# Kernel optimization log

Measured on AMD Instinct MI355X. Metric: run time of the kernel, lower is better.

Reference implementation:

```python
import jax, jax.numpy as jnp
import numpy as np


def _conv(x, w, b, stride):
    y = jax.lax.conv_general_dilated(x, w, (stride, stride), [(1, 1), (1, 1)],
                                     dimension_numbers=('NCHW', 'OIHW', 'NCHW'))
    return y + b[None, :, None, None]


def _prelu(x, a):
    return jnp.where(x >= 0, x, a[None, :, None, None] * x)


def _conv2_block(x, wa, ba, aa, wb, bb, ab):
    # conv2 = stride-2 conv + PReLU, then stride-1 conv + PReLU (RIFE-style)
    x = _prelu(_conv(x, wa, ba, 2), aa)
    return _prelu(_conv(x, wb, bb, 1), ab)


def _halve_flow(flow):
    # F.interpolate(scale_factor=0.5, bilinear, align_corners=False) on exact
    # half-downsampling == 2x2 average pooling; then * 0.5 rescales flow units.
    B, C, H, W = flow.shape
    return flow.reshape(B, C, H // 2, 2, W // 2, 2).mean(axis=(3, 5)) * 0.5


def _splat_one(inp, flow):
    # inp [C,H,W], flow [2,H,W]: bilinear forward-splat (scatter-add) summation
    C, H, W = inp.shape
    gx = jnp.arange(W, dtype=flow.dtype)
    gy = jnp.arange(H, dtype=flow.dtype)
    fx = flow[0] + gx[None, :]  # target x coord per source pixel
    fy = flow[1] + gy[:, None]
    x0 = jnp.floor(fx); y0 = jnp.floor(fy)
    x1 = x0 + 1.0;      y1 = y0 + 1.0
    src = inp.reshape(C, H * W)
    out = jnp.zeros((C, H * W), inp.dtype)
    corners = [(x0, y0, (x1 - fx) * (y1 - fy)),
               (x1, y0, (fx - x0) * (y1 - fy)),
               (x0, y1, (x1 - fx) * (fy - y0)),
               (x1, y1, (fx - x0) * (fy - y0))]
    for xi, yi, w in corners:
        valid = (xi >= 0) & (xi < W) & (yi >= 0) & (yi < H)
        idx = yi.astype(jnp.int32) * W + xi.astype(jnp.int32)
        idx = jnp.where(valid, idx, 0).reshape(-1)
        wv = jnp.where(valid, w, 0.0).reshape(-1)
        out = out.at[:, idx].add(src * wv[None, :])
    return out.reshape(C, H, W)


def _softsplat_avg(inp, flow):
    # strType='average': splat features and a ones channel, divide by count
    num = jax.vmap(_splat_one)(inp, flow)
    cnt = jax.vmap(_splat_one)(jnp.ones_like(inp[:, :1]), flow)
    return num / jnp.where(cnt == 0.0, 1.0, cnt)


def setup_inputs() -> dict:
    key = jax.random.key(0)
    ks = jax.random.split(key, 12)
    B, H, W = 16, 512, 512
    d = {
        'img': jax.random.normal(ks[0], (B, 3, H, W), jnp.float32),
        'flow': jax.random.normal(ks[1], (B, 2, H, W), jnp.float32) * 4.0,
    }
    c = 16
    chans = [(3, c), (c, 2 * c), (2 * c, 4 * c), (4 * c, 8 * c)]
    for i, (ci, co) in enumerate(chans, start=1):
        ka, kb = jax.random.split(ks[1 + i], 2)
        d[f'w{i}a'] = jax.random.normal(ka, (co, ci, 3, 3), jnp.float32) * 0.1
        d[f'b{i}a'] = jnp.zeros((co,), jnp.float32)
        d[f'a{i}a'] = jnp.full((co,), 0.25, jnp.float32)
        d[f'w{i}b'] = jax.random.normal(kb, (co, co, 3, 3), jnp.float32) * 0.1
        d[f'b{i}b'] = jnp.zeros((co,), jnp.float32)
        d[f'a{i}b'] = jnp.full((co,), 0.25, jnp.float32)
    return d


def reference(img, flow,
              w1a, b1a, a1a, w1b, b1b, a1b,
              w2a, b2a, a2a, w2b, b2b, a2b,
              w3a, b3a, a3a, w3b, b3b, a3b,
              w4a, b4a, a4a, w4b, b4b, a4b):
    blocks = [(w1a, b1a, a1a, w1b, b1b, a1b),
              (w2a, b2a, a2a, w2b, b2b, a2b),
              (w3a, b3a, a3a, w3b, b3b, a3b),
              (w4a, b4a, a4a, w4b, b4b, a4b)]
    feat = img
    fl = flow
    pyr = []
    for blk in blocks:
        feat = _conv2_block(feat, *blk)
        fl = _halve_flow(fl)
        pyr.append(_softsplat_avg(feat, fl))
    return tuple(pyr)
```

## Files before the change

### kernel.cpp

```cpp
#include <hip/hip_runtime.h>

#define CDIV(a, b) (((a) + (b) - 1) / (b))

typedef float __attribute__((ext_vector_type(2))) f32x2;
typedef float __attribute__((ext_vector_type(4))) f32x4;

__device__ __forceinline__ void pk_fma(f32x2& d, f32x2 a, f32x2 b) {
    asm("v_pk_fma_f32 %0, %1, %2, %0" : "+v"(d) : "v"(a), "v"(b));
}

__device__ __forceinline__ void fadd_native(float* p, float v) {
    unsafeAtomicAdd(p, v);
}

template <int STRIDE, int TW, int TH, int CB>
__global__ __launch_bounds__(256)
void conv3x3_pk_kernel(const float* __restrict__ in,
                       const float* __restrict__ wgt,
                       const float* __restrict__ bias,
                       const float* __restrict__ alpha,
                       float* __restrict__ out,
                       int Ci, int Hi, int Wi, int Co, int Ho, int Wo,
                       int nTX) {
    constexpr int KO  = 16;
    constexpr int PX  = TW / 16, PY = TH / 16;
    constexpr int ISX = TW * STRIDE + 2;
    constexpr int ISY = TH * STRIDE + 2;
    constexpr int ISS = ISX * ISY;
    constexpr int NST = (CB * ISS + 255) / 256;
    constexpr int NWT = (CB * 9 * KO + 255) / 256;
    __shared__ float s_in[CB * ISS];
    __shared__ __align__(16) float s_wt[CB * 9 * KO];

    const int b   = blockIdx.z;
    const int co0 = blockIdx.y * KO;
    const int tX  = (blockIdx.x % nTX) * TW;
    const int tY  = (blockIdx.x / nTX) * TH;
    const int t   = threadIdx.x;
    const int tcx = t & 15, tcy = t >> 4;
    const int ox0 = PX * tcx, oy0 = PY * tcy;
    const int HiWi = Hi * Wi;

    int  poff[NST];
    bool pval[NST];
    const int ix0 = tX * STRIDE - 1, iy0 = tY * STRIDE - 1;
#pragma unroll
    for (int s = 0; s < NST; ++s) {
        const int i = t + s * 256;
        int off = 0; bool v = false;
        if (i < CB * ISS) {
            const int p = i / ISS, j = i - p * ISS;
            const int r = j / ISX, c = j - r * ISX;
            const int gy = iy0 + r, gx = ix0 + c;
            v = (gy >= 0) && (gy < Hi) && (gx >= 0) && (gx < Wi);
            off = v ? (p * HiWi + gy * Wi + gx) : 0;
        }
        poff[s] = off; pval[s] = v;
    }
    int  wofs[NWT], wdst[NWT];
    bool wvs[NWT];
#pragma unroll
    for (int s = 0; s < NWT; ++s) {
        const int j = t + s * 256;
        bool v = j < CB * 9 * KO;
        int ofs = 0, dst = 0;
        if (v) {
            const int p = j / (9 * KO), rem = j - p * 9 * KO;
            const int k = rem / KO, ko = rem - k * KO;
            ofs = ((co0 + ko) * Ci + p) * 9 + k;
            dst = (p * 9 + k) * KO + ko;
        }
        wofs[s] = ofs; wdst[s] = dst; wvs[s] = v;
    }

    f32x2 acc2[KO / 2][PY][PX];
#pragma unroll
    for (int cp = 0; cp < KO / 2; ++cp)
#pragma unroll
        for (int dy = 0; dy < PY; ++dy)
#pragma unroll
            for (int dx = 0; dx < PX; ++dx) acc2[cp][dy][dx] = (f32x2){0.f, 0.f};

    const float* inb = in + (size_t)b * Ci * HiWi;

    float rs[NST], rw[NWT];
#pragma unroll
    for (int s = 0; s < NST; ++s) rs[s] = pval[s] ? inb[poff[s]] : 0.f;
#pragma unroll
    for (int s = 0; s < NWT; ++s) rw[s] = wvs[s] ? wgt[wofs[s]] : 0.f;

    const int bx = ox0 * STRIDE, by = oy0 * STRIDE;

    for (int ci = 0; ci < Ci; ci += CB) {
        __syncthreads();
#pragma unroll
        for (int s = 0; s < NST; ++s) {
            const int i = t + s * 256;
            if (i < CB * ISS) s_in[i] = rs[s];
        }
#pragma unroll
        for (int s = 0; s < NWT; ++s)
            if (wvs[s]) s_wt[wdst[s]] = rw[s];
        if (ci + CB < Ci) {
            const float* nb = inb + (size_t)(ci + CB) * HiWi;
            const int w9 = (ci + CB) * 9;
#pragma unroll
            for (int s = 0; s < NST; ++s) rs[s] = pval[s] ? nb[poff[s]] : 0.f;
#pragma unroll
            for (int s = 0; s < NWT; ++s)
                rw[s] = wvs[s] ? wgt[wofs[s] + w9] : 0.f;
        }
        __syncthreads();

#pragma unroll
        for (int p = 0; p < CB; ++p) {
            const float* sp = s_in + p * ISS;
#pragma unroll
            for (int ky = 0; ky < 3; ++ky)
#pragma unroll
                for (int kx = 0; kx < 3; ++kx) {
                    const int k = ky * 3 + kx;
                    f32x2 t2[PY][PX];
#pragma unroll
                    for (int dy = 0; dy < PY; ++dy)
#pragma unroll
                        for (int dx = 0; dx < PX; ++dx) {
                            const float tv =
                                sp[(by + dy * STRIDE + ky) * ISX + bx +
                                   dx * STRIDE + kx];
                            t2[dy][dx] = (f32x2){tv, tv};
                        }
                    const float* wb = s_wt + (p * 9 + k) * KO;
#pragma unroll
                    for (int kq = 0; kq < KO / 4; ++kq) {
                        const f32x4 w4 =
                            *reinterpret_cast<const f32x4*>(wb + 4 * kq);
                        const f32x2 wlo = {w4[0], w4[1]};
                        const f32x2 whi = {w4[2], w4[3]};
#pragma unroll
                        for (int dy = 0; dy < PY; ++dy)
#pragma unroll
                            for (int dx = 0; dx < PX; ++dx) {
                                pk_fma(acc2[2 * kq][dy][dx], t2[dy][dx], wlo);
                                pk_fma(acc2[2 * kq + 1][dy][dx], t2[dy][dx], whi);
                            }
                    }
                }
        }
    }

#pragma unroll
    for (int cp = 0; cp < KO / 2; ++cp)
#pragma unroll
        for (int h = 0; h < 2; ++h) {
            const int co = co0 + 2 * cp + h;
            const float bv = bias[co], av = alpha[co];
#pragma unroll
            for (int dy = 0; dy < PY; ++dy) {
                const int oy = tY + oy0 + dy;
#pragma unroll
                for (int dx = 0; dx < PX; ++dx) {
                    const int ox = tX + ox0 + dx;
                    float v = acc2[cp][dy][dx][h] + bv;
                    v = v >= 0.f ? v : av * v;
                    out[(((size_t)b * Co + co) * Ho + oy) * Wo + ox] = v;
                }
            }
        }
}

__global__ void halve_flow_kernel(const float* __restrict__ in,
                                  float* __restrict__ out,
                                  int BC, int Ho, int Wo, int Hi, int Wi) {
    const int idx = blockIdx.x * blockDim.x + threadIdx.x;
    const int total = BC * Ho * Wo;
    if (idx >= total) return;
    const int wo = idx % Wo;
    int t = idx / Wo;
    const int ho = t % Ho;
    const int bc = t / Ho;
    const float* p = in + ((size_t)bc * Hi + 2 * ho) * Wi + 2 * wo;
    out[idx] = (p[0] + p[1] + p[Wi] + p[Wi + 1]) * 0.125f;
}

__global__ void splat_outlier_kernel(const float* __restrict__ feat,
                                     const float* __restrict__ flow,
                                     float* __restrict__ num,
                                     float* __restrict__ cnt,
                                     int* __restrict__ flag,
                                     int B, int C, int H, int W, float thr) {
    const int HW = H * W;
    const int idx = blockIdx.x * blockDim.x + threadIdx.x;
    if (idx >= B * HW) return;
    const int b = idx / HW, px = idx - b * HW;
    const int y = px / W, x = px - y * W;
    const float dx = flow[(size_t)b * 2 * HW + px];
    const float dy = flow[(size_t)b * 2 * HW + HW + px];
    if (fabsf(dx) <= thr && fabsf(dy) <= thr) return;
    atomicAdd(flag, 1);
    const float fx = dx + (float)x, fy = dy + (float)y;
    const float x0f = floorf(fx), y0f = floorf(fy);
    const int x0 = (int)x0f, y0 = (int)y0f;
    const float ax = fx - x0f, ay = fy - y0f;
    const float w[4] = {(1.f - ax) * (1.f - ay), ax * (1.f - ay),
                        (1.f - ax) * ay,         ax * ay};
    const int cx[4] = {x0, x0 + 1, x0, x0 + 1};
    const int cy[4] = {y0, y0, y0 + 1, y0 + 1};
    float* cb = cnt + (size_t)b * HW;
    for (int k = 0; k < 4; ++k) {
        if (cx[k] < 0 || cx[k] >= W || cy[k] < 0 || cy[k] >= H) continue;
        if (w[k] == 0.f) continue;
        const size_t d = (size_t)cy[k] * W + cx[k];
        fadd_native(cb + d, w[k]);
        for (int c = 0; c < C; ++c)
            fadd_native(num + ((size_t)b * C + c) * HW + d,
                        feat[((size_t)b * C + c) * HW + px] * w[k]);
    }
}

template <int TS, int K, int NCH, int HCAP>
__global__ __launch_bounds__(256)
void splat_gather_kernel(const float* __restrict__ feat,
                         const float* __restrict__ flow,
                         const float* __restrict__ cnt_ov,
                         const int* __restrict__ oflag,
                         float* __restrict__ out,
                         int C, int H, int W, int nTX) {
    constexpr int WS   = TS + 2 * K;
    constexpr int SSTR = WS + 1;
    constexpr int RUN  = TS * TS / 256;
    constexpr int TPR  = TS / RUN;
    constexpr float THR = (float)(K - 1);
    __shared__ float s_fx[WS * SSTR];
    __shared__ float s_fy[WS * SSTR];
    __shared__ unsigned short s_hit[256 * HCAP];

    const int b   = blockIdx.z;
    const int c0  = blockIdx.y * NCH;
    const int tx0 = (blockIdx.x % nTX) * TS;
    const int ty0 = (blockIdx.x / nTX) * TS;
    const int t   = threadIdx.x;
    const int HW  = H * W;
    const float* flx = flow + (size_t)b * 2 * HW;
    const float* fly = flx + HW;
    const float* fb  = feat + ((size_t)b * C + c0) * HW;

    for (int i = t; i < WS * WS; i += 256) {
        const int wsy = i / WS, wsx = i - wsy * WS;
        const int gy = ty0 - K + wsy, gx = tx0 - K + wsx;
        float fxr = 1e9f, fyr = 1e9f;
        if (gy >= 0 && gy < H && gx >= 0 && gx < W) {
            const float dxf = flx[(size_t)gy * W + gx];
            const float dyf = fly[(size_t)gy * W + gx];
            if (fabsf(dxf) <= THR && fabsf(dyf) <= THR) {
                fxr = dxf + (float)(gx - tx0);
                fyr = dyf + (float)(gy - ty0);
            }
        }
        s_fx[wsy * SSTR + wsx] = fxr;
        s_fy[wsy * SSTR + wsx] = fyr;
    }
    __syncthreads();

    const int r  = t / TPR;
    const int x0 = (t % TPR) * RUN;

    int n = 0;
    unsigned short* hl = s_hit + t * HCAP;
#pragma unroll
    for (int dy = 0; dy <= 2 * K; ++dy) {
        const int wsy = r + dy;
        const int base = wsy * SSTR + x0;
#pragma unroll
        for (int dxx = 0; dxx < RUN + 2 * K; ++dxx) {
            const float fyr = s_fy[base + dxx];
            const float fxr = s_fx[base + dxx];
            const float ty = fyr - (float)r;
            const float ux = fxr - (float)x0;
            if (ty > -1.f && ty < 1.f && ux > -1.f && ux < (float)RUN &&
                n < HCAP) {
                hl[n] = (unsigned short)((wsy << 6) | (x0 + dxx));
                ++n;
            }
        }
    }

    float acc[RUN][NCH];
    float cnt[RUN];
#pragma unroll
    for (int m = 0; m < RUN; ++m) {
        cnt[m] = 0.f;
#pragma unroll
        for (int ch = 0; ch < NCH; ++ch) acc[m][ch] = 0.f;
    }

    for (int k = 0; k < n; ++k) {
        const int idx = hl[k];
        const int wsy = idx >> 6, wsx = idx & 63;
        const float fxr = s_fx[wsy * SSTR + wsx];
        const float fyr = s_fy[wsy * SSTR + wsx];
        const float wy = 1.f - fabsf(fyr - (float)r);
        const float ux = fxr - (float)x0;
        const int gsy = ty0 - K + wsy, gsx = tx0 - K + wsx;
        const float* fp = fb + (size_t)gsy * W + gsx;
        float wm[RUN];
#pragma unroll
        for (int m = 0; m < RUN; ++m) {
            wm[m] = fmaxf(0.f, 1.f - fabsf(ux - (float)m)) * wy;
            cnt[m] += wm[m];
        }
#pragma unroll
        for (int ch = 0; ch < NCH; ++ch) {
            const float f = fp[(size_t)ch * HW];
#pragma unroll
            for (int m = 0; m < RUN; ++m)
                acc[m][ch] = fmaf(wm[m], f, acc[m][ch]);
        }
    }

    const int has = *oflag;
    const int gy = ty0 + r;
    const size_t rowoff = (size_t)gy * W + (tx0 + x0);
    float inv[RUN];
#pragma unroll
    for (int m = 0; m < RUN; ++m) {
        float cv = cnt[m];
        if (has) cv += cnt_ov[(size_t)b * HW + rowoff + m];
        inv[m] = 1.f / ((cv == 0.f) ? 1.f : cv);
    }
#pragma unroll
    for (int ch = 0; ch < NCH; ++ch) {
        const size_t go = ((size_t)b * C + (c0 + ch)) * HW + rowoff;
        if constexpr (RUN == 4) {
            float vv[4];
#pragma unroll
            for (int m = 0; m < 4; ++m) {
                float x = acc[m][ch];
                if (has) x += out[go + m];
                vv[m] = x * inv[m];
            }
            float4 v4 = {vv[0], vv[1], vv[2], vv[3]};
            *reinterpret_cast<float4*>(out + go) = v4;
        } else {
            float x = acc[0][ch];
            if (has) x += out[go];
            out[go] = x * inv[0];
        }
    }
}

extern "C" void kernel_launch(void* const* d_in, const int* in_sizes, int n_in,
                              void* d_out, int out_size, void* d_ws, size_t ws_size,
                              hipStream_t stream) {
    (void)in_sizes; (void)n_in; (void)ws_size;

    const float* img  = (const float*)d_in[0];
    const float* flow = (const float*)d_in[1];
    const float* P[4][6];
    for (int i = 0; i < 4; ++i)
        for (int j = 0; j < 6; ++j)
            P[i][j] = (const float*)d_in[2 + 6 * i + j];

    const int Bn = 16;
    float* ws = (float*)d_ws;
    float* bufA = ws;
    float* bufB = ws + 16777216;
    float* flA  = ws + 33554432;
    float* flB  = ws + 35651584;
    float* cnt  = ws + 36175872;
    int*   flag = (int*)(ws + 37224448);
    float* out  = (float*)d_out;

    hipMemsetAsync(d_out, 0, (size_t)out_size * sizeof(float), stream);

    auto halve = [&](const float* in, float* o, int Hi, int Wi) {
        const int Ho = Hi / 2, Wo = Wi / 2;
        const int total = Bn * 2 * Ho * Wo;
        hipLaunchKernelGGL(halve_flow_kernel, dim3(CDIV(total, 256)), dim3(256),
                           0, stream, in, o, Bn * 2, Ho, Wo, Hi, Wi);
    };

    float* p1 = out;
    float* p2 = p1 + (size_t)Bn * 16 * 256 * 256;
    float* p3 = p2 + (size_t)Bn * 32 * 128 * 128;
    float* p4 = p3 + (size_t)Bn * 64 * 64 * 64;

#define CONV(S, TWv, THv, CBv, inp, wi, o, Ci_, Hi_, Wi_, Co_)                 \
    do {                                                                       \
        const int Ho_ = (Hi_) / (S), Wo_ = (Wi_) / (S);                        \
        const int nTX_ = Wo_ / (TWv), nTY_ = Ho_ / (THv);                      \
        hipLaunchKernelGGL((conv3x3_pk_kernel<S, TWv, THv, CBv>),              \
                           dim3(nTX_ * nTY_, (Co_) / 16, Bn), dim3(256), 0,    \
                           stream, inp, P[wi][0 + 3 * ((S) == 1)],             \
                           P[wi][1 + 3 * ((S) == 1)], P[wi][2 + 3 * ((S) == 1)],\
                           o, Ci_, Hi_, Wi_, Co_, Ho_, Wo_, nTX_);             \
    } while (0)

    CONV(2, 32, 32, 1, img,  0, bufA, 3, 512, 512, 16);
    CONV(1, 32, 32, 2, bufA, 0, bufB, 16, 256, 256, 16);
    halve(flow, flA, 512, 512);
    {
        const int C = 16, H = 256, W = 256;
        hipMemsetAsync(cnt, 0, (size_t)Bn * H * W * sizeof(float), stream);
        hipMemsetAsync(flag, 0, sizeof(int), stream);
        hipLaunchKernelGGL(splat_outlier_kernel, dim3(CDIV(Bn * H * W, 256)),
                           dim3(256), 0, stream, bufB, flA, p1, cnt, flag,
                           Bn, C, H, W, 3.f);
        hipLaunchKernelGGL((splat_gather_kernel<32, 4, 16, 40>),
                           dim3((W / 32) * (H / 32), C / 16, Bn), dim3(256), 0,
                           stream, bufB, flA, cnt, flag, p1, C, H, W, W / 32);
    }

    CONV(2, 32, 32, 1, bufB, 1, bufA, 16, 256, 256, 32);
    CONV(1, 32, 32, 2, bufA, 1, bufB, 32, 128, 128, 32);
    halve(flA, flB, 256, 256);
    {
        const int C = 32, H = 128, W = 128;
        hipMemsetAsync(cnt, 0, (size_t)Bn * H * W * sizeof(float), stream);
        hipMemsetAsync(flag, 0, sizeof(int), stream);
        hipLaunchKernelGGL(splat_outlier_kernel, dim3(CDIV(Bn * H * W, 256)),
                           dim3(256), 0, stream, bufB, flB, p2, cnt, flag,
                           Bn, C, H, W, 2.f);
        hipLaunchKernelGGL((splat_gather_kernel<32, 3, 16, 40>),
                           dim3((W / 32) * (H / 32), C / 16, Bn), dim3(256), 0,
                           stream, bufB, flB, cnt, flag, p2, C, H, W, W / 32);
    }

    CONV(2, 32, 16, 1, bufB, 2, bufA, 32, 128, 128, 64);
    CONV(1, 32, 16, 2, bufA, 2, bufB, 64, 64, 64, 64);
    halve(flB, flA, 128, 128);
    {
        const int C = 64, H = 64, W = 64;
        hipMemsetAsync(cnt, 0, (size_t)Bn * H * W * sizeof(float), stream);
        hipMemsetAsync(flag, 0, sizeof(int), stream);
        hipLaunchKernelGGL(splat_outlier_kernel, dim3(CDIV(Bn * H * W, 256)),
                           dim3(256), 0, stream, bufB, flA, p3, cnt, flag,
                           Bn, C, H, W, 1.f);
        hipLaunchKernelGGL((splat_gather_kernel<16, 2, 16, 24>),
                           dim3((W / 16) * (H / 16), C / 16, Bn), dim3(256), 0,
                           stream, bufB, flA, cnt, flag, p3, C, H, W, W / 16);
    }

    CONV(2, 16, 16, 1, bufB, 3, bufA, 64, 64, 64, 128);
    CONV(1, 16, 16, 2, bufA, 3, bufB, 128, 32, 32, 128);
    halve(flA, flB, 64, 64);
    {
        const int C = 128, H = 32, W = 32;
        hipMemsetAsync(cnt, 0, (size_t)Bn * H * W * sizeof(float), stream);
        hipMemsetAsync(flag, 0, sizeof(int), stream);
        hipLaunchKernelGGL(splat_outlier_kernel, dim3(CDIV(Bn * H * W, 256)),
                           dim3(256), 0, stream, bufB, flB, p4, cnt, flag,
                           Bn, C, H, W, 1.f);
        hipLaunchKernelGGL((splat_gather_kernel<16, 2, 16, 24>),
                           dim3((W / 16) * (H / 16), C / 16, Bn), dim3(256), 0,
                           stream, bufB, flB, cnt, flag, p4, C, H, W, W / 16);
    }
#undef CONV
}
```

Before: 1.173 ms.

## Stage feature tiles in LDS per channel and drop global outlier flag

The gather splat kernel now loads each channel's feature window into shared memory, double-buffered through registers with a prefetch of the next channel. It then accumulates per channel from LDS rather than issuing scattered global loads for every hit and channel. Flow x/y are packed into one interleaved float2 shared array, the global atomic outlier flag is replaced by a per-pixel check on the count value, and hit-list capacities are reduced. This trades register-heavy accumulators for two barriers per channel and a redo of the hit-list loop for each channel.

```diff
diff --git a/kernel.cpp b/kernel.cpp
--- a/kernel.cpp
+++ b/kernel.cpp
@@ -187,7 +187,6 @@
                                      const float* __restrict__ flow,
                                      float* __restrict__ num,
                                      float* __restrict__ cnt,
-                                     int* __restrict__ flag,
                                      int B, int C, int H, int W, float thr) {
     const int HW = H * W;
     const int idx = blockIdx.x * blockDim.x + threadIdx.x;
@@ -197,7 +196,6 @@
     const float dx = flow[(size_t)b * 2 * HW + px];
     const float dy = flow[(size_t)b * 2 * HW + HW + px];
     if (fabsf(dx) <= thr && fabsf(dy) <= thr) return;
-    atomicAdd(flag, 1);
     const float fx = dx + (float)x, fy = dy + (float)y;
     const float x0f = floorf(fx), y0f = floorf(fy);
     const int x0 = (int)x0f, y0 = (int)y0f;
@@ -220,19 +218,19 @@
 
 template <int TS, int K, int NCH, int HCAP>
 __global__ __launch_bounds__(256)
-void splat_gather_kernel(const float* __restrict__ feat,
-                         const float* __restrict__ flow,
-                         const float* __restrict__ cnt_ov,
-                         const int* __restrict__ oflag,
-                         float* __restrict__ out,
-                         int C, int H, int W, int nTX) {
+void splat_gather2_kernel(const float* __restrict__ feat,
+                          const float* __restrict__ flow,
+                          const float* __restrict__ cnt_ov,
+                          float* __restrict__ out,
+                          int C, int H, int W, int nTX) {
     constexpr int WS   = TS + 2 * K;
     constexpr int SSTR = WS + 1;
     constexpr int RUN  = TS * TS / 256;
     constexpr int TPR  = TS / RUN;
+    constexpr int NSF  = (WS * WS + 255) / 256;
     constexpr float THR = (float)(K - 1);
-    __shared__ float s_fx[WS * SSTR];
-    __shared__ float s_fy[WS * SSTR];
+    __shared__ __align__(8) float s_xy[2 * WS * SSTR];
+    __shared__ float s_feat[WS * SSTR];
     __shared__ unsigned short s_hit[256 * HCAP];
 
     const int b   = blockIdx.z;
@@ -245,20 +243,30 @@
     const float* fly = flx + HW;
     const float* fb  = feat + ((size_t)b * C + c0) * HW;
 
-    for (int i = t; i < WS * WS; i += 256) {
-        const int wsy = i / WS, wsx = i - wsy * WS;
-        const int gy = ty0 - K + wsy, gx = tx0 - K + wsx;
-        float fxr = 1e9f, fyr = 1e9f;
-        if (gy >= 0 && gy < H && gx >= 0 && gx < W) {
-            const float dxf = flx[(size_t)gy * W + gx];
-            const float dyf = fly[(size_t)gy * W + gx];
-            if (fabsf(dxf) <= THR && fabsf(dyf) <= THR) {
-                fxr = dxf + (float)(gx - tx0);
-                fyr = dyf + (float)(gy - ty0);
-            }
-        }
-        s_fx[wsy * SSTR + wsx] = fxr;
-        s_fy[wsy * SSTR + wsx] = fyr;
+    int  foff[NSF], sdst[NSF];
+    bool fval[NSF];
+#pragma unroll
+    for (int s = 0; s < NSF; ++s) {
+        const int i = t + s * 256;
+        foff[s] = 0; sdst[s] = 0; fval[s] = false;
+        if (i < WS * WS) {
+            const int wsy = i / WS, wsx = i - wsy * WS;
+            const int gy = ty0 - K + wsy, gx = tx0 - K + wsx;
+            const int off = wsy * SSTR + wsx;
+            sdst[s] = off;
+            float fxr = 1e9f, fyr = 1e9f;
+            if (gy >= 0 && gy < H && gx >= 0 && gx < W) {
+                fval[s] = true;
+                foff[s] = gy * W + gx;
+                const float dxf = flx[foff[s]];
+                const float dyf = fly[foff[s]];
+                if (fabsf(dxf) <= THR && fabsf(dyf) <= THR) {
+                    fxr = dxf + (float)(gx - tx0);
+                    fyr = dyf + (float)(gy - ty0);
+                }
+            }
+            *reinterpret_cast<f32x2*>(&s_xy[2 * off]) = (f32x2){fxr, fyr};
+        }
     }
     __syncthreads();
 
@@ -273,10 +281,10 @@
         const int base = wsy * SSTR + x0;
 #pragma unroll
         for (int dxx = 0; dxx < RUN + 2 * K; ++dxx) {
-            const float fyr = s_fy[base + dxx];
-            const float fxr = s_fx[base + dxx];
-            const float ty = fyr - (float)r;
-            const float ux = fxr - (float)x0;
+            const f32x2 xy =
+                *reinterpret_cast<const f32x2*>(&s_xy[2 * (base + dxx)]);
+            const float ty = xy[1] - (float)r;
+            const float ux = xy[0] - (float)x0;
             if (ty > -1.f && ty < 1.f && ux > -1.f && ux < (float)RUN &&
                 n < HCAP) {
                 hl[n] = (unsigned short)((wsy << 6) | (x0 + dxx));
@@ -285,65 +293,71 @@
         }
     }
 
-    float acc[RUN][NCH];
-    float cnt[RUN];
-#pragma unroll
-    for (int m = 0; m < RUN; ++m) {
-        cnt[m] = 0.f;
-#pragma unroll
-        for (int ch = 0; ch < NCH; ++ch) acc[m][ch] = 0.f;
-    }
-
-    for (int k = 0; k < n; ++k) {
-        const int idx = hl[k];
-        const int wsy = idx >> 6, wsx = idx & 63;
-        const float fxr = s_fx[wsy * SSTR + wsx];
-        const float fyr = s_fy[wsy * SSTR + wsx];
-        const float wy = 1.f - fabsf(fyr - (float)r);
-        const float ux = fxr - (float)x0;
-        const int gsy = ty0 - K + wsy, gsx = tx0 - K + wsx;
-        const float* fp = fb + (size_t)gsy * W + gsx;
-        float wm[RUN];
-#pragma unroll
-        for (int m = 0; m < RUN; ++m) {
-            wm[m] = fmaxf(0.f, 1.f - fabsf(ux - (float)m)) * wy;
-            cnt[m] += wm[m];
-        }
-#pragma unroll
-        for (int ch = 0; ch < NCH; ++ch) {
-            const float f = fp[(size_t)ch * HW];
-#pragma unroll
-            for (int m = 0; m < RUN; ++m)
-                acc[m][ch] = fmaf(wm[m], f, acc[m][ch]);
-        }
-    }
-
-    const int has = *oflag;
-    const int gy = ty0 + r;
-    const size_t rowoff = (size_t)gy * W + (tx0 + x0);
+    const int gyd = ty0 + r;
+    const size_t rowoff = (size_t)gyd * W + (tx0 + x0);
+    float cv_ov[RUN];
+#pragma unroll
+    for (int m = 0; m < RUN; ++m)
+        cv_ov[m] = cnt_ov[(size_t)b * HW + rowoff + m];
+
+    float rs[NSF];
+#pragma unroll
+    for (int s = 0; s < NSF; ++s) rs[s] = fval[s] ? fb[foff[s]] : 0.f;
+
     float inv[RUN];
 #pragma unroll
-    for (int m = 0; m < RUN; ++m) {
-        float cv = cnt[m];
-        if (has) cv += cnt_ov[(size_t)b * HW + rowoff + m];
-        inv[m] = 1.f / ((cv == 0.f) ? 1.f : cv);
-    }
-#pragma unroll
     for (int ch = 0; ch < NCH; ++ch) {
+        __syncthreads();
+#pragma unroll
+        for (int s = 0; s < NSF; ++s)
+            if (t + s * 256 < WS * WS) s_feat[sdst[s]] = rs[s];
+        if (ch + 1 < NCH) {
+            const float* nfb = fb + (size_t)(ch + 1) * HW;
+#pragma unroll
+            for (int s = 0; s < NSF; ++s) rs[s] = fval[s] ? nfb[foff[s]] : 0.f;
+        }
+        __syncthreads();
+
+        float a[RUN];
+        float cw[RUN];
+#pragma unroll
+        for (int m = 0; m < RUN; ++m) { a[m] = 0.f; cw[m] = 0.f; }
+        for (int k = 0; k < n; ++k) {
+            const int idx = hl[k];
+            const int off = (idx >> 6) * SSTR + (idx & 63);
+            const f32x2 xy = *reinterpret_cast<const f32x2*>(&s_xy[2 * off]);
+            const float f = s_feat[off];
+            const float wy = 1.f - fabsf(xy[1] - (float)r);
+            const float ux = xy[0] - (float)x0;
+#pragma unroll
+            for (int m = 0; m < RUN; ++m) {
+                const float wm = fmaxf(0.f, 1.f - fabsf(ux - (float)m)) * wy;
+                a[m] = fmaf(wm, f, a[m]);
+                if (ch == 0) cw[m] += wm;
+            }
+        }
+        if (ch == 0) {
+#pragma unroll
+            for (int m = 0; m < RUN; ++m) {
+                const float cv = cw[m] + cv_ov[m];
+                inv[m] = 1.f / ((cv == 0.f) ? 1.f : cv);
+            }
+        }
+
         const size_t go = ((size_t)b * C + (c0 + ch)) * HW + rowoff;
         if constexpr (RUN == 4) {
             float vv[4];
 #pragma unroll
             for (int m = 0; m < 4; ++m) {
-                float x = acc[m][ch];
-                if (has) x += out[go + m];
+                float x = a[m];
+                if (cv_ov[m] != 0.f) x += out[go + m];
                 vv[m] = x * inv[m];
             }
             float4 v4 = {vv[0], vv[1], vv[2], vv[3]};
             *reinterpret_cast<float4*>(out + go) = v4;
         } else {
-            float x = acc[0][ch];
-            if (has) x += out[go];
+            float x = a[0];
+            if (cv_ov[0] != 0.f) x += out[go];
             out[go] = x * inv[0];
         }
     }
@@ -368,7 +382,6 @@
     float* flA  = ws + 33554432;
     float* flB  = ws + 35651584;
     float* cnt  = ws + 36175872;
-    int*   flag = (int*)(ws + 37224448);
     float* out  = (float*)d_out;
 
     hipMemsetAsync(d_out, 0, (size_t)out_size * sizeof(float), stream);
@@ -396,64 +409,40 @@
                            o, Ci_, Hi_, Wi_, Co_, Ho_, Wo_, nTX_);             \
     } while (0)
 
+#define SPLAT(TSv, Kv, NCHv, HCAPv, featp, flp, op, C_, H_, W_, thr)           \
+    do {                                                                       \
+        hipMemsetAsync(cnt, 0, (size_t)Bn * (H_) * (W_) * sizeof(float),       \
+                       stream);                                                \
+        hipLaunchKernelGGL(splat_outlier_kernel,                               \
+                           dim3(CDIV(Bn * (H_) * (W_), 256)), dim3(256), 0,    \
+                           stream, featp, flp, op, cnt, Bn, C_, H_, W_, thr);  \
+        hipLaunchKernelGGL((splat_gather2_kernel<TSv, Kv, NCHv, HCAPv>),       \
+                           dim3(((W_) / (TSv)) * ((H_) / (TSv)),               \
+                                (C_) / (NCHv), Bn),                            \
+                           dim3(256), 0, stream, featp, flp, cnt, op,          \
+                           C_, H_, W_, (W_) / (TSv));                          \
+    } while (0)
+
     CONV(2, 32, 32, 1, img,  0, bufA, 3, 512, 512, 16);
     CONV(1, 32, 32, 2, bufA, 0, bufB, 16, 256, 256, 16);
     halve(flow, flA, 512, 512);
-    {
-        const int C = 16, H = 256, W = 256;
-        hipMemsetAsync(cnt, 0, (size_t)Bn * H * W * sizeof(float), stream);
-        hipMemsetAsync(flag, 0, sizeof(int), stream);
-        hipLaunchKernelGGL(splat_outlier_kernel, dim3(CDIV(Bn * H * W, 256)),
-                           dim3(256), 0, stream, bufB, flA, p1, cnt, flag,
-                           Bn, C, H, W, 3.f);
-        hipLaunchKernelGGL((splat_gather_kernel<32, 4, 16, 40>),
-                           dim3((W / 32) * (H / 32), C / 16, Bn), dim3(256), 0,
-                           stream, bufB, flA, cnt, flag, p1, C, H, W, W / 32);
-    }
+    SPLAT(32, 4, 16, 32, bufB, flA, p1, 16, 256, 256, 3.f);
 
     CONV(2, 32, 32, 1, bufB, 1, bufA, 16, 256, 256, 32);
     CONV(1, 32, 32, 2, bufA, 1, bufB, 32, 128, 128, 32);
     halve(flA, flB, 256, 256);
-    {
-        const int C = 32, H = 128, W = 128;
-        hipMemsetAsync(cnt, 0, (size_t)Bn * H * W * sizeof(float), stream);
-        hipMemsetAsync(flag, 0, sizeof(int), stream);
-        hipLaunchKernelGGL(splat_outlier_kernel, dim3(CDIV(Bn * H * W, 256)),
-                           dim3(256), 0, stream, bufB, flB, p2, cnt, flag,
-                           Bn, C, H, W, 2.f);
-        hipLaunchKernelGGL((splat_gather_kernel<32, 3, 16, 40>),
-                           dim3((W / 32) * (H / 32), C / 16, Bn), dim3(256), 0,
-                           stream, bufB, flB, cnt, flag, p2, C, H, W, W / 32);
-    }
+    SPLAT(32, 3, 16, 32, bufB, flB, p2, 32, 128, 128, 2.f);
 
     CONV(2, 32, 16, 1, bufB, 2, bufA, 32, 128, 128, 64);
     CONV(1, 32, 16, 2, bufA, 2, bufB, 64, 64, 64, 64);
     halve(flB, flA, 128, 128);
-    {
-        const int C = 64, H = 64, W = 64;
-        hipMemsetAsync(cnt, 0, (size_t)Bn * H * W * sizeof(float), stream);
-        hipMemsetAsync(flag, 0, sizeof(int), stream);
-        hipLaunchKernelGGL(splat_outlier_kernel, dim3(CDIV(Bn * H * W, 256)),
-                           dim3(256), 0, stream, bufB, flA, p3, cnt, flag,
-                           Bn, C, H, W, 1.f);
-        hipLaunchKernelGGL((splat_gather_kernel<16, 2, 16, 24>),
-                           dim3((W / 16) * (H / 16), C / 16, Bn), dim3(256), 0,
-                           stream, bufB, flA, cnt, flag, p3, C, H, W, W / 16);
-    }
+    SPLAT(16, 2, 16, 16, bufB, flA, p3, 64, 64, 64, 1.f);
 
     CONV(2, 16, 16, 1, bufB, 3, bufA, 64, 64, 64, 128);
     CONV(1, 16, 16, 2, bufA, 3, bufB, 128, 32, 32, 128);
     halve(flA, flB, 64, 64);
-    {
-        const int C = 128, H = 32, W = 32;
-        hipMemsetAsync(cnt, 0, (size_t)Bn * H * W * sizeof(float), stream);
-        hipMemsetAsync(flag, 0, sizeof(int), stream);
-        hipLaunchKernelGGL(splat_outlier_kernel, dim3(CDIV(Bn * H * W, 256)),
-                           dim3(256), 0, stream, bufB, flB, p4, cnt, flag,
-                           Bn, C, H, W, 1.f);
-        hipLaunchKernelGGL((splat_gather_kernel<16, 2, 16, 24>),
-                           dim3((W / 16) * (H / 16), C / 16, Bn), dim3(256), 0,
-                           stream, bufB, flB, cnt, flag, p4, C, H, W, W / 16);
-    }
+    SPLAT(16, 2, 16, 16, bufB, flB, p4, 128, 32, 32, 1.f);
+
 #undef CONV
-}
+#undef SPLAT
+}
```

After: 1.023 ms. 1.15x faster.
